# Kernel optimization log

Hardware: AMD Instinct MI355X
Metric: run time of the kernel (lower is better)

Reference implementation:

```python
import jax, jax.numpy as jnp
import numpy as np
import math

B, S, HID = 2, 2048, 1024
NH, HD = 16, 64  # num_heads, head_dim = HID // NH


def setup_inputs() -> dict:
    key = jax.random.key(0)
    ks = jax.random.split(key, 12)
    sc = 1.0 / math.sqrt(HID)
    inp = {
        "x": jax.random.normal(ks[0], (B, S, HID), dtype=jnp.float32),
        "time_deltas": jax.random.uniform(ks[1], (B, S), dtype=jnp.float32),
        # torch.nn.Linear weights are [out, in]; y = x @ W.T + b
        "Wq": jax.random.normal(ks[2], (HID, HID), dtype=jnp.float32) * sc,
        "bq": jnp.zeros((HID,), dtype=jnp.float32),
        "Wk": jax.random.normal(ks[3], (HID, HID), dtype=jnp.float32) * sc,
        "bk": jnp.zeros((HID,), dtype=jnp.float32),
        "Wv": jax.random.normal(ks[4], (HID, HID), dtype=jnp.float32) * sc,
        "bv": jnp.zeros((HID,), dtype=jnp.float32),
        "Wo": jax.random.normal(ks[5], (HID, HID), dtype=jnp.float32) * sc,
        "bo": jnp.zeros((HID,), dtype=jnp.float32),
        "time_decay": jnp.ones((NH,), dtype=jnp.float32),
    }
    return inp


def reference(x, time_deltas, Wq, bq, Wk, bk, Wv, bv, Wo, bo, time_decay):
    b, s, _ = x.shape

    def heads(W, bias):
        # [b, s, hid] -> [b, nh, s, hd]
        return (x @ W.T + bias).reshape(b, s, NH, HD).transpose(0, 2, 1, 3)

    q = heads(Wq, bq)
    k = heads(Wk, bk)
    v = heads(Wv, bv)

    scores = jnp.einsum("bhqd,bhkd->bhqk", q, k) / math.sqrt(HD)

    # pairwise |t_i - t_j| decay bias, per-head learned rate
    tm = jnp.abs(time_deltas[:, :, None] - time_deltas[:, None, :])  # [b, s, s]
    decay = jnp.exp(-time_decay[None, :, None, None] * tm[:, None, :, :])
    scores = scores * decay

    causal = jnp.triu(jnp.ones((s, s), dtype=bool), k=1)  # True above diagonal
    scores = jnp.where(causal[None, None], -jnp.inf, scores)

    attn = jax.nn.softmax(scores, axis=-1)  # dropout is identity at inference
    out = jnp.einsum("bhqk,bhkd->bhqd", attn, v)
    out = out.transpose(0, 2, 1, 3).reshape(b, s, HID)
    return out @ Wo.T + bo
```

## Files before the change

### kernel.cpp

```cpp
#include <hip/hip_runtime.h>
#include <hip/hip_bf16.h>

typedef __attribute__((ext_vector_type(4))) float f32x4;
typedef __attribute__((ext_vector_type(8))) __bf16 bf16x8;
typedef __attribute__((ext_vector_type(4))) unsigned short us4;

static constexpr int BB = 2, SS = 2048, HID = 1024, NH = 16, HD = 64;
static constexpr int M_TOT = BB * SS;

static __device__ __forceinline__ f32x4 mfma16(bf16x8 a, bf16x8 b, f32x4 c) {
  return __builtin_amdgcn_mfma_f32_16x16x32_bf16(a, b, c, 0, 0, 0);
}

static __device__ __forceinline__ unsigned short f2b(float x) {
  __hip_bfloat16 h = __float2bfloat16(x);
  unsigned short u;
  __builtin_memcpy(&u, &h, 2);
  return u;
}

__global__ void cvt_kernel(const float* __restrict__ src,
                           unsigned short* __restrict__ dst, int n4) {
  int idx = blockIdx.x * blockDim.x + threadIdx.x;
  int stride = gridDim.x * blockDim.x;
  const f32x4* s = (const f32x4*)src;
  us4* d = (us4*)dst;
  for (int i = idx; i < n4; i += stride) {
    f32x4 v = s[i];
    us4 o;
    o.x = f2b(v.x); o.y = f2b(v.y); o.z = f2b(v.z); o.w = f2b(v.w);
    d[i] = o;
  }
}

__global__ void cvt_w4(const float* __restrict__ s0, const float* __restrict__ s1,
                       const float* __restrict__ s2, const float* __restrict__ s3,
                       unsigned short* __restrict__ d0, unsigned short* __restrict__ d1,
                       unsigned short* __restrict__ d2, unsigned short* __restrict__ d3,
                       int n4) {
  const float* s; unsigned short* d;
  int z = blockIdx.y;
  if (z == 0)      { s = s0; d = d0; }
  else if (z == 1) { s = s1; d = d1; }
  else if (z == 2) { s = s2; d = d2; }
  else             { s = s3; d = d3; }
  int idx = blockIdx.x * blockDim.x + threadIdx.x;
  int stride = gridDim.x * blockDim.x;
  const f32x4* sv = (const f32x4*)s;
  us4* dv = (us4*)d;
  for (int i = idx; i < n4; i += stride) {
    f32x4 v = sv[i];
    us4 o;
    o.x = f2b(v.x); o.y = f2b(v.y); o.z = f2b(v.z); o.w = f2b(v.w);
    dv[i] = o;
  }
}

static __device__ __forceinline__ void gemm_mainloop(
    const unsigned short* __restrict__ gA,
    const unsigned short* __restrict__ gB,
    unsigned short* As, unsigned short* Bs, int t, f32x4 acc[4][4]) {
  const int l = t & 63;
  const int lr = l & 15, lg = (l >> 4) & 3;
  const int w = t >> 6;
  const int wr = w >> 1, wc = w & 1;
  for (int k0 = 0; k0 < HID; k0 += 64) {
#pragma unroll
    for (int i_ = 0; i_ < 4; ++i_) {
      int chunk = i_ * 256 + t;
      int row = chunk >> 3;
      int col = (chunk & 7) << 3;
      __builtin_amdgcn_global_load_lds(
          (const __attribute__((address_space(1))) unsigned int*)(gA + (size_t)row * HID + k0 + col),
          (__attribute__((address_space(3))) unsigned int*)(As + chunk * 8),
          16, 0, 0);
    }
#pragma unroll
    for (int i_ = 0; i_ < 4; ++i_) {
      int chunk = i_ * 256 + t;
      int row = chunk >> 3;
      int col = (chunk & 7) << 3;
      __builtin_amdgcn_global_load_lds(
          (const __attribute__((address_space(1))) unsigned int*)(gB + (size_t)row * HID + k0 + col),
          (__attribute__((address_space(3))) unsigned int*)(Bs + chunk * 8),
          16, 0, 0);
    }
    __syncthreads();
#pragma unroll
    for (int kk = 0; kk < 2; ++kk) {
      bf16x8 a[4], bb[4];
#pragma unroll
      for (int mf = 0; mf < 4; ++mf)
        a[mf] = *(const bf16x8*)&As[(wr * 64 + mf * 16 + lr) * 64 + kk * 32 + lg * 8];
#pragma unroll
      for (int nf = 0; nf < 4; ++nf)
        bb[nf] = *(const bf16x8*)&Bs[(wc * 64 + nf * 16 + lr) * 64 + kk * 32 + lg * 8];
#pragma unroll
      for (int mf = 0; mf < 4; ++mf)
#pragma unroll
        for (int nf = 0; nf < 4; ++nf)
          acc[mf][nf] = mfma16(a[mf], bb[nf], acc[mf][nf]);
    }
    __syncthreads();
  }
}

__global__ __launch_bounds__(256, 2) void qkv_gemm(
    const unsigned short* __restrict__ xb,
    const unsigned short* __restrict__ wqb, const unsigned short* __restrict__ wkb,
    const unsigned short* __restrict__ wvb,
    const float* __restrict__ bq, const float* __restrict__ bk, const float* __restrict__ bv,
    unsigned short* __restrict__ qo, unsigned short* __restrict__ ko,
    unsigned short* __restrict__ vto) {
  __shared__ unsigned short As[128 * 64];
  __shared__ unsigned short Bs[128 * 64];
  int t = threadIdx.x;
  int z = blockIdx.z;
  const unsigned short* Bmat = (z == 0) ? wqb : (z == 1) ? wkb : wvb;
  const float* bias = (z == 0) ? bq : (z == 1) ? bk : bv;
  int m0 = blockIdx.y * 128, n0 = blockIdx.x * 128;
  f32x4 acc[4][4] = {};
  gemm_mainloop(xb + (size_t)m0 * HID, Bmat + (size_t)n0 * HID, As, Bs, t, acc);

  int l = t & 63, lr = l & 15, lg = (l >> 4) & 3;
  int w = t >> 6, wr = w >> 1, wc = w & 1;
  float scale = (z == 0) ? 0.125f : 1.0f;
#pragma unroll
  for (int nf = 0; nf < 4; ++nf) {
    int n = n0 + wc * 64 + nf * 16 + lr;
    float bs = bias[n];
    int h = n >> 6, d = n & 63;
#pragma unroll
    for (int mf = 0; mf < 4; ++mf) {
#pragma unroll
      for (int j = 0; j < 4; ++j) {
        int m = m0 + wr * 64 + mf * 16 + lg * 4 + j;
        int b = m >> 11, sidx = m & (SS - 1);
        float val = (acc[mf][nf][j] + bs) * scale;
        unsigned short ob = f2b(val);
        if (z == 2)
          vto[((size_t)(b * NH + h) * HD + d) * SS + sidx] = ob;
        else {
          unsigned short* dst = (z == 0) ? qo : ko;
          dst[((size_t)(b * NH + h) * SS + sidx) * HD + d] = ob;
        }
      }
    }
  }
}

__global__ __launch_bounds__(256, 2) void out_gemm(
    const unsigned short* __restrict__ Ab,
    const unsigned short* __restrict__ Wb,
    const float* __restrict__ bias,
    float* __restrict__ C) {
  __shared__ unsigned short As[128 * 64];
  __shared__ unsigned short Bs[128 * 64];
  int t = threadIdx.x;
  int m0 = blockIdx.y * 128, n0 = blockIdx.x * 128;
  f32x4 acc[4][4] = {};
  gemm_mainloop(Ab + (size_t)m0 * HID, Wb + (size_t)n0 * HID, As, Bs, t, acc);

  int l = t & 63, lr = l & 15, lg = (l >> 4) & 3;
  int w = t >> 6, wr = w >> 1, wc = w & 1;
#pragma unroll
  for (int nf = 0; nf < 4; ++nf) {
    int n = n0 + wc * 64 + nf * 16 + lr;
    float bs = bias[n];
#pragma unroll
    for (int mf = 0; mf < 4; ++mf) {
#pragma unroll
      for (int j = 0; j < 4; ++j) {
        int m = m0 + wr * 64 + mf * 16 + lg * 4 + j;
        C[(size_t)m * HID + n] = acc[mf][nf][j] + bs;
      }
    }
  }
}

static __device__ __forceinline__ void stage_kv(
    const unsigned short* __restrict__ kp, const unsigned short* __restrict__ vp,
    int kv0, unsigned short* Kd, unsigned short* Vd, int t) {
#pragma unroll
  for (int i_ = 0; i_ < 2; ++i_) {
    int chunk = i_ * 256 + t;
    int row = chunk >> 3;
    int srcc = ((chunk & 7) ^ (row & 7)) << 3;
    __builtin_amdgcn_global_load_lds(
        (const __attribute__((address_space(1))) unsigned int*)(kp + (size_t)(kv0 + row) * HD + srcc),
        (__attribute__((address_space(3))) unsigned int*)(Kd + chunk * 8), 16, 0, 0);
    __builtin_amdgcn_global_load_lds(
        (const __attribute__((address_space(1))) unsigned int*)(vp + (size_t)row * SS + kv0 + srcc),
        (__attribute__((address_space(3))) unsigned int*)(Vd + chunk * 8), 16, 0, 0);
  }
}

__global__ __launch_bounds__(256, 2) void attn_kernel(
    const unsigned short* __restrict__ qg,
    const unsigned short* __restrict__ kg,
    const unsigned short* __restrict__ vtg,
    const float* __restrict__ td,
    const float* __restrict__ decay,
    unsigned short* __restrict__ outb) {
  __shared__ unsigned short Ks[2][64 * 64];
  __shared__ unsigned short Vs[2][64 * 64];
  __shared__ unsigned short Pl[4][16][68];
  const int t = threadIdx.x;
  const int l = t & 63;
  const int w = t >> 6;
  const int lr = l & 15, lg = (l >> 4) & 3;
  const int L = blockIdx.x;
  const int W = (L & 7) * 64 + (L >> 3);
  const int xp = W & 15;
  const int h = (W >> 4) & 15;
  const int b = W >> 8;
  const unsigned short* qp = qg + ((size_t)(b * NH + h) * SS) * HD;
  const unsigned short* kp = kg + ((size_t)(b * NH + h) * SS) * HD;
  const unsigned short* vp = vtg + ((size_t)(b * NH + h) * HD) * SS;
  const float* tdb = td + (size_t)b * SS;
  const float dec = decay[h];

  for (int seg = 0; seg < 2; ++seg) {
    const int qb = seg ? 31 - xp : xp;
    const int q0 = qb * 64;
    const int qw = q0 + w * 16;

    bf16x8 qf0 = *(const bf16x8*)&qp[(size_t)(qw + lr) * HD + lg * 8];
    bf16x8 qf1 = *(const bf16x8*)&qp[(size_t)(qw + lr) * HD + 32 + lg * 8];
    float tq[4], eq[4], fq[4];
#pragma unroll
    for (int j = 0; j < 4; ++j) {
      tq[j] = tdb[qw + lg * 4 + j];
      eq[j] = __expf(dec * tq[j]);
      fq[j] = __expf(-dec * tq[j]);
    }
    float mrow[4] = {-__builtin_inff(), -__builtin_inff(), -__builtin_inff(), -__builtin_inff()};
    float lsum[4] = {0.f, 0.f, 0.f, 0.f};
    f32x4 o[4] = {};

    stage_kv(kp, vp, 0, Ks[0], Vs[0], t);
    int cur = 0;
    for (int tkv = 0; tkv <= qb; ++tkv) {
      const int kv0 = tkv * 64;
      if (tkv < qb) {
        stage_kv(kp, vp, kv0 + 64, Ks[cur ^ 1], Vs[cur ^ 1], t);
        asm volatile("s_waitcnt vmcnt(4)" ::: "memory");
      } else {
        asm volatile("s_waitcnt vmcnt(0)" ::: "memory");
      }
      __builtin_amdgcn_s_barrier();
      asm volatile("" ::: "memory");
      const unsigned short* Kc = Ks[cur];
      const unsigned short* Vc = Vs[cur];

      f32x4 s[4];
#pragma unroll
      for (int nf = 0; nf < 4; ++nf) {
        int r = nf * 16 + lr;
        bf16x8 kf0 = *(const bf16x8*)&Kc[r * 64 + ((lg ^ (r & 7)) << 3)];
        bf16x8 kf1 = *(const bf16x8*)&Kc[r * 64 + (((4 + lg) ^ (r & 7)) << 3)];
        f32x4 zz = {};
        zz = mfma16(qf0, kf0, zz);
        s[nf] = mfma16(qf1, kf1, zz);
      }
#pragma unroll
      for (int nf = 0; nf < 4; ++nf) {
        int col = kv0 + nf * 16 + lr;
        float tk = tdb[col];
        float ek = __expf(dec * tk);
        float fk = __expf(-dec * tk);
#pragma unroll
        for (int j = 0; j < 4; ++j) {
          int row = qw + lg * 4 + j;
          float wgt = fminf(eq[j] * fk, fq[j] * ek);
          float sv = s[nf][j] * wgt;
          s[nf][j] = (col <= row) ? sv : -__builtin_inff();
        }
      }
#pragma unroll
      for (int j = 0; j < 4; ++j) {
        float x = fmaxf(fmaxf(s[0][j], s[1][j]), fmaxf(s[2][j], s[3][j]));
        x = fmaxf(x, __shfl_xor(x, 1, 16));
        x = fmaxf(x, __shfl_xor(x, 2, 16));
        x = fmaxf(x, __shfl_xor(x, 4, 16));
        x = fmaxf(x, __shfl_xor(x, 8, 16));
        float nm = fmaxf(mrow[j], x);
        float sc = __expf(mrow[j] - nm);
        mrow[j] = nm;
        float rs = 0.f;
#pragma unroll
        for (int nf = 0; nf < 4; ++nf) {
          float pv = __expf(s[nf][j] - nm);
          rs += pv;
          Pl[w][lg * 4 + j][nf * 16 + lr] = f2b(pv);
        }
        rs += __shfl_xor(rs, 1, 16);
        rs += __shfl_xor(rs, 2, 16);
        rs += __shfl_xor(rs, 4, 16);
        rs += __shfl_xor(rs, 8, 16);
        lsum[j] = lsum[j] * sc + rs;
#pragma unroll
        for (int df = 0; df < 4; ++df) o[df][j] *= sc;
      }
#pragma unroll
      for (int kk = 0; kk < 2; ++kk) {
        bf16x8 pa = *(const bf16x8*)&Pl[w][lr][kk * 32 + lg * 8];
        int g = kk * 4 + lg;
#pragma unroll
        for (int df = 0; df < 4; ++df) {
          int r = df * 16 + lr;
          bf16x8 vf = *(const bf16x8*)&Vc[r * 64 + ((g ^ (r & 7)) << 3)];
          o[df] = mfma16(pa, vf, o[df]);
        }
      }
      __syncthreads();
      cur ^= 1;
    }
#pragma unroll
    for (int df = 0; df < 4; ++df) {
#pragma unroll
      for (int j = 0; j < 4; ++j) {
        int srow = qw + lg * 4 + j;
        float val = o[df][j] / lsum[j];
        outb[((size_t)b * SS + srow) * HID + h * HD + df * 16 + lr] = f2b(val);
      }
    }
  }
}

extern "C" void kernel_launch(void* const* d_in, const int* in_sizes, int n_in,
                              void* d_out, int out_size, void* d_ws, size_t ws_size,
                              hipStream_t stream) {
  const float* x    = (const float*)d_in[0];
  const float* td   = (const float*)d_in[1];
  const float* Wq   = (const float*)d_in[2];
  const float* bq   = (const float*)d_in[3];
  const float* Wk   = (const float*)d_in[4];
  const float* bk   = (const float*)d_in[5];
  const float* Wv   = (const float*)d_in[6];
  const float* bv   = (const float*)d_in[7];
  const float* Wo   = (const float*)d_in[8];
  const float* bo   = (const float*)d_in[9];
  const float* tdec = (const float*)d_in[10];
  float* out = (float*)d_out;

  char* ws = (char*)d_ws;
  unsigned short* xb  = (unsigned short*)ws; ws += (size_t)M_TOT * HID * 2;
  unsigned short* wqb = (unsigned short*)ws; ws += (size_t)HID * HID * 2;
  unsigned short* wkb = (unsigned short*)ws; ws += (size_t)HID * HID * 2;
  unsigned short* wvb = (unsigned short*)ws; ws += (size_t)HID * HID * 2;
  unsigned short* wob = (unsigned short*)ws; ws += (size_t)HID * HID * 2;
  unsigned short* qb  = (unsigned short*)ws; ws += (size_t)M_TOT * HID * 2;
  unsigned short* kb  = (unsigned short*)ws; ws += (size_t)M_TOT * HID * 2;
  unsigned short* vtb = (unsigned short*)ws; ws += (size_t)M_TOT * HID * 2;
  unsigned short* ob  = (unsigned short*)ws; ws += (size_t)M_TOT * HID * 2;

  cvt_kernel<<<1024, 256, 0, stream>>>(x, xb, M_TOT * HID / 4);
  cvt_w4<<<dim3(512, 4), 256, 0, stream>>>(Wq, Wk, Wv, Wo, wqb, wkb, wvb, wob, HID * HID / 4);
  qkv_gemm<<<dim3(HID / 128, M_TOT / 128, 3), 256, 0, stream>>>(
      xb, wqb, wkb, wvb, bq, bk, bv, qb, kb, vtb);
  attn_kernel<<<512, 256, 0, stream>>>(qb, kb, vtb, td, tdec, ob);
  out_gemm<<<dim3(HID / 128, M_TOT / 128), 256, 0, stream>>>(ob, wob, bo, out);
}
```

Before: 238.7 us.

## Split attention into one q-block per workgroup, use exp2 and mask only diagonal

The attention kernel previously had each workgroup process a paired short and long q-block in sequence. Now it launches 1024 workgroups with one q-block each, ordered longest first, and raises launch_bounds occupancy to 4. Exponentials are rewritten in base 2 with log2(e) folded into the decay factors, and the causal mask is applied only on the diagonal tile. The P staging buffer drops its padding in favour of an XOR swizzle. The intent is better occupancy and load balance and less per-element ALU work, at the risk of register pressure from the higher occupancy bound.

```diff
diff --git a/kernel.cpp b/kernel.cpp
--- a/kernel.cpp
+++ b/kernel.cpp
@@ -17,6 +17,10 @@
   unsigned short u;
   __builtin_memcpy(&u, &h, 2);
   return u;
+}
+
+static __device__ __forceinline__ float ex2(float x) {
+  return __builtin_amdgcn_exp2f(x);
 }
 
 __global__ void cvt_kernel(const float* __restrict__ src,
@@ -195,7 +199,7 @@
   }
 }
 
-__global__ __launch_bounds__(256, 2) void attn_kernel(
+__global__ __launch_bounds__(256, 4) void attn_kernel(
     const unsigned short* __restrict__ qg,
     const unsigned short* __restrict__ kg,
     const unsigned short* __restrict__ vtg,
@@ -204,126 +208,132 @@
     unsigned short* __restrict__ outb) {
   __shared__ unsigned short Ks[2][64 * 64];
   __shared__ unsigned short Vs[2][64 * 64];
-  __shared__ unsigned short Pl[4][16][68];
+  __shared__ unsigned short Pl[4][16][64];
   const int t = threadIdx.x;
   const int l = t & 63;
   const int w = t >> 6;
   const int lr = l & 15, lg = (l >> 4) & 3;
   const int L = blockIdx.x;
-  const int W = (L & 7) * 64 + (L >> 3);
-  const int xp = W & 15;
-  const int h = (W >> 4) & 15;
-  const int b = W >> 8;
+  const int W = (L & 7) * 128 + (L >> 3);
+  const int bh = W >> 5;
+  const int qb = 31 - (W & 31);
+  const int h = bh & 15, b = bh >> 4;
   const unsigned short* qp = qg + ((size_t)(b * NH + h) * SS) * HD;
   const unsigned short* kp = kg + ((size_t)(b * NH + h) * SS) * HD;
   const unsigned short* vp = vtg + ((size_t)(b * NH + h) * HD) * SS;
   const float* tdb = td + (size_t)b * SS;
   const float dec = decay[h];
-
-  for (int seg = 0; seg < 2; ++seg) {
-    const int qb = seg ? 31 - xp : xp;
-    const int q0 = qb * 64;
-    const int qw = q0 + w * 16;
-
-    bf16x8 qf0 = *(const bf16x8*)&qp[(size_t)(qw + lr) * HD + lg * 8];
-    bf16x8 qf1 = *(const bf16x8*)&qp[(size_t)(qw + lr) * HD + 32 + lg * 8];
-    float tq[4], eq[4], fq[4];
-#pragma unroll
-    for (int j = 0; j < 4; ++j) {
-      tq[j] = tdb[qw + lg * 4 + j];
-      eq[j] = __expf(dec * tq[j]);
-      fq[j] = __expf(-dec * tq[j]);
-    }
-    float mrow[4] = {-__builtin_inff(), -__builtin_inff(), -__builtin_inff(), -__builtin_inff()};
-    float lsum[4] = {0.f, 0.f, 0.f, 0.f};
-    f32x4 o[4] = {};
-
-    stage_kv(kp, vp, 0, Ks[0], Vs[0], t);
-    int cur = 0;
-    for (int tkv = 0; tkv <= qb; ++tkv) {
-      const int kv0 = tkv * 64;
-      if (tkv < qb) {
-        stage_kv(kp, vp, kv0 + 64, Ks[cur ^ 1], Vs[cur ^ 1], t);
-        asm volatile("s_waitcnt vmcnt(4)" ::: "memory");
-      } else {
-        asm volatile("s_waitcnt vmcnt(0)" ::: "memory");
-      }
-      __builtin_amdgcn_s_barrier();
-      asm volatile("" ::: "memory");
-      const unsigned short* Kc = Ks[cur];
-      const unsigned short* Vc = Vs[cur];
-
-      f32x4 s[4];
-#pragma unroll
-      for (int nf = 0; nf < 4; ++nf) {
-        int r = nf * 16 + lr;
-        bf16x8 kf0 = *(const bf16x8*)&Kc[r * 64 + ((lg ^ (r & 7)) << 3)];
-        bf16x8 kf1 = *(const bf16x8*)&Kc[r * 64 + (((4 + lg) ^ (r & 7)) << 3)];
-        f32x4 zz = {};
-        zz = mfma16(qf0, kf0, zz);
-        s[nf] = mfma16(qf1, kf1, zz);
-      }
+  const float L2E = 1.44269504f;
+  const float dl = dec * L2E;
+
+  const int q0 = qb * 64;
+  const int qw = q0 + w * 16;
+
+  bf16x8 qf0 = *(const bf16x8*)&qp[(size_t)(qw + lr) * HD + lg * 8];
+  bf16x8 qf1 = *(const bf16x8*)&qp[(size_t)(qw + lr) * HD + 32 + lg * 8];
+  float tq[4], eqL[4], fqL[4];
+#pragma unroll
+  for (int j = 0; j < 4; ++j) {
+    tq[j] = tdb[qw + lg * 4 + j];
+    eqL[j] = ex2(dl * tq[j]) * L2E;
+    fqL[j] = ex2(-dl * tq[j]) * L2E;
+  }
+  float mrow[4] = {-__builtin_inff(), -__builtin_inff(), -__builtin_inff(), -__builtin_inff()};
+  float lsum[4] = {0.f, 0.f, 0.f, 0.f};
+  f32x4 o[4] = {};
+
+  stage_kv(kp, vp, 0, Ks[0], Vs[0], t);
+  int cur = 0;
+  for (int tkv = 0; tkv <= qb; ++tkv) {
+    const int kv0 = tkv * 64;
+    if (tkv < qb) {
+      stage_kv(kp, vp, kv0 + 64, Ks[cur ^ 1], Vs[cur ^ 1], t);
+      asm volatile("s_waitcnt vmcnt(4)" ::: "memory");
+    } else {
+      asm volatile("s_waitcnt vmcnt(0)" ::: "memory");
+    }
+    __builtin_amdgcn_s_barrier();
+    asm volatile("" ::: "memory");
+    const unsigned short* Kc = Ks[cur];
+    const unsigned short* Vc = Vs[cur];
+
+    f32x4 s[4];
+#pragma unroll
+    for (int nf = 0; nf < 4; ++nf) {
+      int r = nf * 16 + lr;
+      bf16x8 kf0 = *(const bf16x8*)&Kc[r * 64 + ((lg ^ (r & 7)) << 3)];
+      bf16x8 kf1 = *(const bf16x8*)&Kc[r * 64 + (((4 + lg) ^ (r & 7)) << 3)];
+      f32x4 zz = {};
+      zz = mfma16(qf0, kf0, zz);
+      s[nf] = mfma16(qf1, kf1, zz);
+    }
+#pragma unroll
+    for (int nf = 0; nf < 4; ++nf) {
+      float tk = tdb[kv0 + nf * 16 + lr];
+      float ek = ex2(dl * tk);
+      float fk = ex2(-dl * tk);
+#pragma unroll
+      for (int j = 0; j < 4; ++j)
+        s[nf][j] *= fminf(eqL[j] * fk, fqL[j] * ek);
+    }
+    if (tkv == qb) {
 #pragma unroll
       for (int nf = 0; nf < 4; ++nf) {
         int col = kv0 + nf * 16 + lr;
-        float tk = tdb[col];
-        float ek = __expf(dec * tk);
-        float fk = __expf(-dec * tk);
 #pragma unroll
         for (int j = 0; j < 4; ++j) {
           int row = qw + lg * 4 + j;
-          float wgt = fminf(eq[j] * fk, fq[j] * ek);
-          float sv = s[nf][j] * wgt;
-          s[nf][j] = (col <= row) ? sv : -__builtin_inff();
+          if (col > row) s[nf][j] = -__builtin_inff();
         }
       }
-#pragma unroll
-      for (int j = 0; j < 4; ++j) {
-        float x = fmaxf(fmaxf(s[0][j], s[1][j]), fmaxf(s[2][j], s[3][j]));
-        x = fmaxf(x, __shfl_xor(x, 1, 16));
-        x = fmaxf(x, __shfl_xor(x, 2, 16));
-        x = fmaxf(x, __shfl_xor(x, 4, 16));
-        x = fmaxf(x, __shfl_xor(x, 8, 16));
-        float nm = fmaxf(mrow[j], x);
-        float sc = __expf(mrow[j] - nm);
-        mrow[j] = nm;
-        float rs = 0.f;
-#pragma unroll
-        for (int nf = 0; nf < 4; ++nf) {
-          float pv = __expf(s[nf][j] - nm);
-          rs += pv;
-          Pl[w][lg * 4 + j][nf * 16 + lr] = f2b(pv);
-        }
-        rs += __shfl_xor(rs, 1, 16);
-        rs += __shfl_xor(rs, 2, 16);
-        rs += __shfl_xor(rs, 4, 16);
-        rs += __shfl_xor(rs, 8, 16);
-        lsum[j] = lsum[j] * sc + rs;
-#pragma unroll
-        for (int df = 0; df < 4; ++df) o[df][j] *= sc;
-      }
-#pragma unroll
-      for (int kk = 0; kk < 2; ++kk) {
-        bf16x8 pa = *(const bf16x8*)&Pl[w][lr][kk * 32 + lg * 8];
-        int g = kk * 4 + lg;
-#pragma unroll
-        for (int df = 0; df < 4; ++df) {
-          int r = df * 16 + lr;
-          bf16x8 vf = *(const bf16x8*)&Vc[r * 64 + ((g ^ (r & 7)) << 3)];
-          o[df] = mfma16(pa, vf, o[df]);
-        }
-      }
-      __syncthreads();
-      cur ^= 1;
-    }
-#pragma unroll
-    for (int df = 0; df < 4; ++df) {
-#pragma unroll
-      for (int j = 0; j < 4; ++j) {
-        int srow = qw + lg * 4 + j;
-        float val = o[df][j] / lsum[j];
-        outb[((size_t)b * SS + srow) * HID + h * HD + df * 16 + lr] = f2b(val);
-      }
+    }
+#pragma unroll
+    for (int j = 0; j < 4; ++j) {
+      float x = fmaxf(fmaxf(s[0][j], s[1][j]), fmaxf(s[2][j], s[3][j]));
+      x = fmaxf(x, __shfl_xor(x, 1, 16));
+      x = fmaxf(x, __shfl_xor(x, 2, 16));
+      x = fmaxf(x, __shfl_xor(x, 4, 16));
+      x = fmaxf(x, __shfl_xor(x, 8, 16));
+      float nm = fmaxf(mrow[j], x);
+      float sc = ex2(mrow[j] - nm);
+      mrow[j] = nm;
+      int row = lg * 4 + j;
+      float rs = 0.f;
+#pragma unroll
+      for (int nf = 0; nf < 4; ++nf) {
+        float pv = ex2(s[nf][j] - nm);
+        rs += pv;
+        Pl[w][row][(nf * 16 + lr) ^ ((row & 7) << 3)] = f2b(pv);
+      }
+      rs += __shfl_xor(rs, 1, 16);
+      rs += __shfl_xor(rs, 2, 16);
+      rs += __shfl_xor(rs, 4, 16);
+      rs += __shfl_xor(rs, 8, 16);
+      lsum[j] = lsum[j] * sc + rs;
+#pragma unroll
+      for (int df = 0; df < 4; ++df) o[df][j] *= sc;
+    }
+#pragma unroll
+    for (int kk = 0; kk < 2; ++kk) {
+      bf16x8 pa = *(const bf16x8*)&Pl[w][lr][(kk * 32 + lg * 8) ^ ((lr & 7) << 3)];
+      int g = kk * 4 + lg;
+#pragma unroll
+      for (int df = 0; df < 4; ++df) {
+        int r = df * 16 + lr;
+        bf16x8 vf = *(const bf16x8*)&Vc[r * 64 + ((g ^ (r & 7)) << 3)];
+        o[df] = mfma16(pa, vf, o[df]);
+      }
+    }
+    __syncthreads();
+    cur ^= 1;
+  }
+#pragma unroll
+  for (int df = 0; df < 4; ++df) {
+#pragma unroll
+    for (int j = 0; j < 4; ++j) {
+      int srow = qw + lg * 4 + j;
+      float val = o[df][j] / lsum[j];
+      outb[((size_t)b * SS + srow) * HID + h * HD + df * 16 + lr] = f2b(val);
     }
   }
 }
@@ -359,6 +369,6 @@
   cvt_w4<<<dim3(512, 4), 256, 0, stream>>>(Wq, Wk, Wv, Wo, wqb, wkb, wvb, wob, HID * HID / 4);
   qkv_gemm<<<dim3(HID / 128, M_TOT / 128, 3), 256, 0, stream>>>(
       xb, wqb, wkb, wvb, bq, bk, bv, qb, kb, vtb);
-  attn_kernel<<<512, 256, 0, stream>>>(qb, kb, vtb, td, tdec, ob);
+  attn_kernel<<<1024, 256, 0, stream>>>(qb, kb, vtb, td, tdec, ob);
   out_gemm<<<dim3(HID / 128, M_TOT / 128), 256, 0, stream>>>(ob, wob, bo, out);
 }
```

Measured after the change: 276.7 us. 1.16x slower.
